# Kernel tuning notes

Hardware: AMD Instinct MI355X
Metric: run time of the kernel (lower is better)

## Reference

```python
import jax, jax.numpy as jnp
import numpy as np

N = 50000      # total nodes across batched subgraphs
E = 800000     # total edges
R = 4          # num_relations
G = 16         # number of graphs (questions) in batch
NODE_DIM = 128
QDIM = 768
RQ = 64        # reduced_qn_dim
RN = 64        # reduced_node_dim
H = 128        # hidden_dim
OUT = 64       # output_dim


def setup_inputs() -> dict:
    key = jax.random.key(0)
    ks = jax.random.split(key, 16)
    def lin(k, i, o):
        return jax.random.normal(k, (i, o), jnp.float32) / np.float32(np.sqrt(i))
    def rel(k, i, o):
        return jax.random.normal(k, (R, i, o), jnp.float32) / np.float32(np.sqrt(i))
    return {
        "x": jax.random.normal(ks[0], (N, NODE_DIM), jnp.float32),
        "edge_index": jax.random.randint(ks[1], (2, E), 0, N, dtype=jnp.int32),
        "edge_attr": jax.random.randint(ks[2], (E,), 0, R, dtype=jnp.int32),
        "batch": jnp.sort(jax.random.randint(ks[3], (N,), 0, G, dtype=jnp.int32)),
        "question_embedding": jax.random.normal(ks[4], (G, QDIM), jnp.float32),
        "qn_W": lin(ks[5], QDIM, RQ), "qn_b": jnp.zeros((RQ,), jnp.float32),
        "W0": rel(ks[6], NODE_DIM, RN), "root0": lin(ks[7], NODE_DIM, RN), "b0": jnp.zeros((RN,), jnp.float32),
        "W1": rel(ks[8], RN + RQ, H), "root1": lin(ks[9], RN + RQ, H), "b1": jnp.zeros((H,), jnp.float32),
        "W2": rel(ks[10], H, H), "root2": lin(ks[11], H, H), "b2": jnp.zeros((H,), jnp.float32),
        "W3": rel(ks[12], H, OUT), "root3": lin(ks[13], H, OUT), "b3": jnp.zeros((OUT,), jnp.float32),
    }


def rgcn_conv(x, src, dst, etype, W, root, b):
    """PyG RGCNConv: out_i = x_i @ root + b + sum_r mean_{j in N_r(i)} x_j @ W_r."""
    out = x @ root + b
    for r in range(R):
        h = x @ W[r]                                  # [N, out] transform-then-gather
        mask = (etype == r)
        msgs = jnp.where(mask[:, None], h[src], 0.0)  # [E, out]
        s = jax.ops.segment_sum(msgs, dst, num_segments=N)
        cnt = jax.ops.segment_sum(mask.astype(x.dtype), dst, num_segments=N)
        out = out + s / jnp.maximum(cnt, 1.0)[:, None]
    return out


def reference(x, edge_index, edge_attr, batch, question_embedding,
              qn_W, qn_b, W0, root0, b0, W1, root1, b1, W2, root2, b2, W3, root3, b3):
    src, dst = edge_index[0], edge_index[1]
    q = jax.nn.relu(question_embedding @ qn_W + qn_b)          # [G, RQ]
    h = jax.nn.relu(rgcn_conv(x, src, dst, edge_attr, W0, root0, b0))
    combined = jnp.concatenate([h, q[batch]], axis=1)          # [N, RN+RQ]
    h = jax.nn.relu(rgcn_conv(combined, src, dst, edge_attr, W1, root1, b1))
    h = jax.nn.relu(rgcn_conv(h, src, dst, edge_attr, W2, root2, b2))
    return rgcn_conv(h, src, dst, edge_attr, W3, root3, b3)
```

## Files before the change

kernel.cpp:

```cpp
#include <hip/hip_runtime.h>
#include <hip/hip_bf16.h>

#define NN 50000
#define EE 800000
#define GG 16
#define QD 768
#define NBUCK 196
#define EPB 4000

#define AGG_GRID 2048
#define AGG_STRIDE (AGG_GRID * 4)

typedef __bf16 bf16x8 __attribute__((ext_vector_type(8)));
typedef float f32x4 __attribute__((ext_vector_type(4)));
typedef int v4i __attribute__((ext_vector_type(4)));

extern "C" __device__ int __llvm_amdgcn_raw_buffer_load_i32(v4i rsrc, int voffset,
                                                            int soffset, int aux)
    __asm("llvm.amdgcn.raw.buffer.load.i32");

static __device__ __forceinline__ float bflo(unsigned u) {
    union { unsigned v; float f; } c; c.v = u << 16; return c.f;
}
static __device__ __forceinline__ float bfhi(unsigned u) {
    union { unsigned v; float f; } c; c.v = u & 0xffff0000u; return c.f;
}


#define PB_CVT 6250
#define PB_W0  (PB_CVT + 160)
#define PB_W1  (PB_W0 + 320)
#define PB_W2  (PB_W1 + 320)
#define PB_W3  (PB_W2 + 160)
#define PB_Q   (PB_W3 + 16)
#define PB_Z   (PB_Q + 1)
#define PB_HIST (PB_Z + 256)

__global__ __launch_bounds__(256) void prep_hist(
        const float* __restrict__ x, __hip_bfloat16* __restrict__ xb0e,
        __hip_bfloat16* __restrict__ xb1e,
        const float* __restrict__ qe, const float* __restrict__ qn_W,
        const float* __restrict__ qn_b, float* __restrict__ q,
        const float* __restrict__ W0, const float* __restrict__ root0, __hip_bfloat16* __restrict__ W5T0,
        const float* __restrict__ W1, const float* __restrict__ root1, __hip_bfloat16* __restrict__ W5T1,
        const float* __restrict__ W2, const float* __restrict__ root2, __hip_bfloat16* __restrict__ W5T2,
        const float* __restrict__ W3, const float* __restrict__ root3, __hip_bfloat16* __restrict__ W5T3,
        const int* __restrict__ edst, int* __restrict__ bcnt) {
    __shared__ float red[256];
    int blk = blockIdx.x, tid = threadIdx.x;
    if (blk < PB_CVT) {
        int i = blk * 256 + tid;
        float4 v = ((const float4*)x)[i];
        union { ushort4 u; __hip_bfloat16 h[4]; } o;
        o.h[0] = __float2bfloat16(v.x); o.h[1] = __float2bfloat16(v.y);
        o.h[2] = __float2bfloat16(v.z); o.h[3] = __float2bfloat16(v.w);
        ((ushort4*)xb0e)[i] = o.u;
    } else if (blk < PB_W3) {
        const float* W; const float* root; __hip_bfloat16* WT; int O, base;
        if (blk < PB_W0)      { W = W0; root = root0; WT = W5T0; O = 64;  base = PB_CVT; }
        else if (blk < PB_W1) { W = W1; root = root1; WT = W5T1; O = 128; base = PB_W0; }
        else if (blk < PB_W2) { W = W2; root = root2; WT = W5T2; O = 128; base = PB_W1; }
        else                  { W = W3; root = root3; WT = W5T3; O = 64;  base = PB_W2; }
        int idx = (blk - base) * 256 + tid;
        int o = idx / 640, k = idx - o * 640;
        float v;
        if (k < 128) v = root[(size_t)k * O + o];
        else { int r = (k - 128) >> 7, kk = (k - 128) & 127; v = W[((size_t)r * 128 + kk) * O + o]; }
        WT[idx] = __float2bfloat16(v);
    } else if (blk < PB_Q) {
        int g = blk - PB_W3;
        int o = tid & 63, kc = tid >> 6;
        const float* qr = qe + (size_t)g * QD;
        float s = 0.f;
        int k0 = kc * 192;
        for (int k = k0; k < k0 + 192; ++k)
            s = fmaf(qr[k], qn_W[(size_t)k * 64 + o], s);
        red[tid] = s;
        __syncthreads();
        if (tid < 64) {
            float t = red[tid] + red[tid + 64] + red[tid + 128] + red[tid + 192] + qn_b[o];
            q[g * 64 + o] = fmaxf(t, 0.f);
        }
    } else if (blk < PB_Z) {
        if (tid < 64) {
            ((unsigned*)((char*)xb0e + (size_t)NN * 256))[tid] = 0u;
            ((unsigned*)((char*)xb1e + (size_t)NN * 256))[tid] = 0u;
        }
    } else {
        __shared__ int h[NBUCK];
        int hb = blk - PB_Z;
        for (int i = tid; i < NBUCK; i += 256) h[i] = 0;
        __syncthreads();
        for (int e = hb * 256 + tid; e < EE; e += 256 * 256)
            atomicAdd(&h[edst[e] >> 8], 1);
        __syncthreads();
        for (int i = tid; i < NBUCK; i += 256) if (h[i]) atomicAdd(&bcnt[i], h[i]);
    }
}


__global__ void bucket_scan(const int* __restrict__ bcnt, int* __restrict__ bbase,
                            int* __restrict__ bcur) {
    __shared__ int wt[4];
    int tid = threadIdx.x, lane = tid & 63, w = tid >> 6;
    int v = (tid < NBUCK) ? bcnt[tid] : 0;
    int sc = v;
#pragma unroll
    for (int off = 1; off < 64; off <<= 1) {
        int t = __shfl_up(sc, off, 64);
        if (lane >= off) sc += t;
    }
    if (lane == 63) wt[w] = sc;
    __syncthreads();
    int wbase = 0;
    for (int ww = 0; ww < w; ++ww) wbase += wt[ww];
    int excl = wbase + sc - v;
    if (tid <= NBUCK) bbase[tid] = excl;
    if (tid < NBUCK) bcur[tid] = excl;
}

__global__ __launch_bounds__(256) void bin_edges(const int* __restrict__ src,
                                                 const int* __restrict__ dst,
                                                 const int* __restrict__ et,
                                                 int* __restrict__ bcur,
                                                 unsigned* __restrict__ binned) {
    __shared__ int lcnt[NBUCK];
    __shared__ int lbase[NBUCK];
    int tid = threadIdx.x;
    int e0 = blockIdx.x * EPB, e1 = min(e0 + EPB, EE);
    for (int base = e0; base < e1; base += 2048) {
        for (int i = tid; i < NBUCK; i += 256) lcnt[i] = 0;
        __syncthreads();
        unsigned ent[8]; int bk[8], rk[8];
#pragma unroll
        for (int k = 0; k < 8; ++k) {
            int e = base + k * 256 + tid;
            if (e < e1) {
                int d = dst[e];
                bk[k] = d >> 8;
                ent[k] = ((unsigned)src[e] << 10) | ((unsigned)et[e] << 8) | (unsigned)(d & 255);
                rk[k] = atomicAdd(&lcnt[bk[k]], 1);
            } else bk[k] = -1;
        }
        __syncthreads();
        for (int i = tid; i < NBUCK; i += 256)
            lbase[i] = lcnt[i] ? atomicAdd(&bcur[i], lcnt[i]) : 0;
        __syncthreads();
#pragma unroll
        for (int k = 0; k < 8; ++k)
            if (bk[k] >= 0) binned[lbase[bk[k]] + rk[k]] = ent[k];
        __syncthreads();
    }
}

__global__ __launch_bounds__(256) void csr_fine(const int* __restrict__ bbase,
                                                const unsigned* __restrict__ binned,
                                                int* __restrict__ csr,
                                                int* __restrict__ offsets,
                                                int4* __restrict__ cnt4) {
    __shared__ int cnt[1024];
    __shared__ int wt[4];
    int b = blockIdx.x, tid = threadIdx.x, lane = tid & 63, w = tid >> 6;
    int seg0 = bbase[b], seg1 = bbase[b + 1];
    for (int i = tid; i < 1024; i += 256) cnt[i] = 0;
    __syncthreads();
    for (int e = seg0 + tid; e < seg1; e += 256) {
        unsigned u = binned[e];
        atomicAdd(&cnt[(u & 255) * 4 + ((u >> 8) & 3)], 1);
    }
    __syncthreads();
    int c0 = cnt[tid * 4], c1 = cnt[tid * 4 + 1], c2 = cnt[tid * 4 + 2], c3 = cnt[tid * 4 + 3];
    int s = c0 + c1 + c2 + c3;
    int sc = s;
#pragma unroll
    for (int off = 1; off < 64; off <<= 1) {
        int t = __shfl_up(sc, off, 64);
        if (lane >= off) sc += t;
    }
    if (lane == 63) wt[w] = sc;
    __syncthreads();
    int wbase = 0;
    for (int ww = 0; ww < w; ++ww) wbase += wt[ww];
    int excl = wbase + sc - s;
    cnt[tid * 4]     = excl;
    cnt[tid * 4 + 1] = excl + c0;
    cnt[tid * 4 + 2] = excl + c0 + c1;
    cnt[tid * 4 + 3] = excl + c0 + c1 + c2;
    int node = b * 256 + tid;
    if (node < NN) {
        offsets[node] = seg0 + excl;
        cnt4[node] = make_int4(c0, c1, c2, c3);
    }
    if (b == NBUCK - 1 && tid == 0) offsets[NN] = EE;
    __syncthreads();
    for (int e = seg0 + tid; e < seg1; e += 256) {
        unsigned u = binned[e];
        int r = atomicAdd(&cnt[(u & 255) * 4 + ((u >> 8) & 3)], 1);
        csr[seg0 + r] = (int)(((u >> 10) << 2) | ((u >> 8) & 3));
    }
}


__global__ __launch_bounds__(256) void agg_x(const __hip_bfloat16* __restrict__ X,
                                             const int* __restrict__ offsets,
                                             const int4* __restrict__ cnt4,
                                             const int* __restrict__ csr,
                                             __hip_bfloat16* __restrict__ X5agg) {
    int lane = threadIdx.x & 63;
    int gw = blockIdx.x * 4 + (threadIdx.x >> 6);
    int laneoff = lane * 4;

    v4i rsrc;
    rsrc.x = (int)(unsigned)(size_t)X;
    rsrc.y = (int)((size_t)X >> 32);
    rsrc.z = NN * 256;
    rsrc.w = 0x00020000;

    for (int n0 = gw; n0 < NN; n0 += AGG_STRIDE) {
        int node = __builtin_amdgcn_readfirstlane(n0);
        int e0 = __builtin_amdgcn_readfirstlane(offsets[node]);
        int4 c4 = cnt4[node];
        int cs0 = __builtin_amdgcn_readfirstlane(c4.x);
        int cs1 = __builtin_amdgcn_readfirstlane(c4.y);
        int cs2 = __builtin_amdgcn_readfirstlane(c4.z);
        int cs3 = __builtin_amdgcn_readfirstlane(c4.w);
        int st1 = cs0, st2 = st1 + cs1, st3 = st2 + cs2;
        int maxc = max(max(cs0, cs1), max(cs2, cs3));
        float aL[4] = {0.f, 0.f, 0.f, 0.f}, aH[4] = {0.f, 0.f, 0.f, 0.f};
        for (int base = 0; base < maxc; base += 64) {
            int pk0 = csr[min(e0 + base + lane, EE - 1)];
            int pk1 = csr[min(e0 + st1 + base + lane, EE - 1)];
            int pk2 = csr[min(e0 + st2 + base + lane, EE - 1)];
            int pk3 = csr[min(e0 + st3 + base + lane, EE - 1)];
            int mm = min(64, maxc - base);
            for (int j = 0; j < mm; j += 4) {
                unsigned u[16];
#pragma unroll
                for (int jj = 0; jj < 4; ++jj) {
                    int i = base + j + jj;
                    int sl = j + jj;
                    int s0 = (i < cs0) ? ((__builtin_amdgcn_readlane(pk0, sl) >> 2) << 8) : 0x7F000000;
                    int s1 = (i < cs1) ? ((__builtin_amdgcn_readlane(pk1, sl) >> 2) << 8) : 0x7F000000;
                    int s2 = (i < cs2) ? ((__builtin_amdgcn_readlane(pk2, sl) >> 2) << 8) : 0x7F000000;
                    int s3 = (i < cs3) ? ((__builtin_amdgcn_readlane(pk3, sl) >> 2) << 8) : 0x7F000000;
                    u[jj * 4 + 0] = (unsigned)__llvm_amdgcn_raw_buffer_load_i32(rsrc, laneoff, s0, 0);
                    u[jj * 4 + 1] = (unsigned)__llvm_amdgcn_raw_buffer_load_i32(rsrc, laneoff, s1, 0);
                    u[jj * 4 + 2] = (unsigned)__llvm_amdgcn_raw_buffer_load_i32(rsrc, laneoff, s2, 0);
                    u[jj * 4 + 3] = (unsigned)__llvm_amdgcn_raw_buffer_load_i32(rsrc, laneoff, s3, 0);
                }
#pragma unroll
                for (int k = 0; k < 16; ++k) {
                    int r = k & 3;
                    aL[r] += bflo(u[k]);
                    aH[r] += bfhi(u[k]);
                }
            }
        }
        char* x5 = (char*)X5agg;
        int csa[4] = {cs0, cs1, cs2, cs3};
#pragma unroll
        for (int r = 0; r < 4; ++r) {
            float iv = 1.f / fmaxf((float)csa[r], 1.f);
            __hip_bfloat16 g0 = __float2bfloat16(aL[r] * iv);
            __hip_bfloat16 g1 = __float2bfloat16(aH[r] * iv);
            ushort2 pkd;
            pkd.x = *(unsigned short*)&g0; pkd.y = *(unsigned short*)&g1;
            *(ushort2*)(x5 + (size_t)node * 1024 + r * 256 + lane * 4) = pkd;
        }
    }
}


template <int O, int MODE>
__global__ __launch_bounds__(256) void dense5(const __hip_bfloat16* __restrict__ Xself,
                                              const __hip_bfloat16* __restrict__ X5agg,
                                              const __hip_bfloat16* __restrict__ W5T,
                                              const float* __restrict__ bias,
                                              const float* __restrict__ q,
                                              const int* __restrict__ batch,
                                              __hip_bfloat16* __restrict__ xnext,
                                              float* __restrict__ out) {
    __shared__ char lds[16384];
    constexpr int NCT = O / 16;
    int tid = threadIdx.x;
    int wave = tid >> 6, lane = tid & 63;
    int quad = lane >> 4, l15 = lane & 15;
    int mbase = blockIdx.x * 128 + wave * 32;
    const __bf16* Ws = (const __bf16*)W5T;

    f32x4 acc[2][NCT];
#pragma unroll
    for (int mt = 0; mt < 2; ++mt)
#pragma unroll
        for (int t = 0; t < NCT; ++t) acc[mt][t] = f32x4{0, 0, 0, 0};

    int arow0 = min(mbase + l15, NN - 1);
    int arow1 = min(mbase + 16 + l15, NN - 1);
    const __bf16* aps0 = (const __bf16*)Xself + (size_t)arow0 * 128;
    const __bf16* aps1 = (const __bf16*)Xself + (size_t)arow1 * 128;
    const __bf16* apg0 = (const __bf16*)X5agg + (size_t)arow0 * 512;
    const __bf16* apg1 = (const __bf16*)X5agg + (size_t)arow1 * 512;

    for (int kc = 0; kc < 10; ++kc) {
        int k0 = kc * 64;
        const __bf16* a0base = (kc < 2) ? aps0 + kc * 64 : apg0 + (kc - 2) * 64;
        const __bf16* a1base = (kc < 2) ? aps1 + kc * 64 : apg1 + (kc - 2) * 64;
        __syncthreads();
        constexpr int NF = NCT * 2 * 64;
#pragma unroll
        for (int i = 0; i < NF / 256; ++i) {
            int f = tid + i * 256;
            int fl = f & 63;
            int o = (f >> 7) * 16 + (fl & 15);
            int kk = k0 + ((f >> 6) & 1) * 32 + ((fl >> 4) & 3) * 8;
            *(uint4*)(lds + f * 16) = *(const uint4*)(Ws + (size_t)o * 640 + kk);
        }
        __syncthreads();
#pragma unroll
        for (int ks = 0; ks < 2; ++ks) {
            bf16x8 a0 = *(const bf16x8*)(a0base + ks * 32 + quad * 8);
            bf16x8 a1 = *(const bf16x8*)(a1base + ks * 32 + quad * 8);
#pragma unroll
            for (int t = 0; t < NCT; ++t) {
                bf16x8 b = *(const bf16x8*)(lds + ((t * 2 + ks) * 64 + lane) * 16);
                acc[0][t] = __builtin_amdgcn_mfma_f32_16x16x32_bf16(a0, b, acc[0][t], 0, 0, 0);
                acc[1][t] = __builtin_amdgcn_mfma_f32_16x16x32_bf16(a1, b, acc[1][t], 0, 0, 0);
            }
        }
    }
    __syncthreads();

    if (MODE == 2) {
#pragma unroll
        for (int mt = 0; mt < 2; ++mt)
#pragma unroll
            for (int t = 0; t < NCT; ++t) {
                int col = t * 16 + l15;
                float bv = bias[col];
#pragma unroll
                for (int reg = 0; reg < 4; ++reg) {
                    int row = mbase + mt * 16 + quad * 4 + reg;
                    if (row < NN) out[(size_t)row * 64 + col] = acc[mt][t][reg] + bv;
                }
            }
        return;
    }

    __hip_bfloat16* tp = (__hip_bfloat16*)(lds + wave * 4096);
#pragma unroll
    for (int mt = 0; mt < 2; ++mt) {
        int m0 = mbase + mt * 16;
#pragma unroll
        for (int t = 0; t < NCT; ++t) {
            int col = t * 16 + l15;
            float bv = bias[col];
#pragma unroll
            for (int reg = 0; reg < 4; ++reg)
                tp[(quad * 4 + reg) * 128 + col] =
                    __float2bfloat16(fmaxf(acc[mt][t][reg] + bv, 0.f));
        }
        if (MODE == 0) {
            int row = lane >> 2;
            int cs = (lane & 3) * 16;
            int rnode = min(m0 + row, NN - 1);
            int g = batch[rnode];
#pragma unroll
            for (int i = 0; i < 4; ++i) {
                float4 v = *(const float4*)(q + g * 64 + cs + i * 4);
                __hip_bfloat16 q0 = __float2bfloat16(v.x), q1 = __float2bfloat16(v.y);
                __hip_bfloat16 q2 = __float2bfloat16(v.z), q3 = __float2bfloat16(v.w);
                ushort4 pk;
                pk.x = *(unsigned short*)&q0; pk.y = *(unsigned short*)&q1;
                pk.z = *(unsigned short*)&q2; pk.w = *(unsigned short*)&q3;
                *(ushort4*)(tp + row * 128 + 64 + cs + i * 4) = pk;
            }
        }
#pragma unroll
        for (int p = 0; p < 4; ++p) {
            int c = p * 64 + lane;
            int row = m0 + (c >> 4);
            if (row < NN)
                *(uint4*)((char*)xnext + (size_t)row * 256 + (c & 15) * 16) =
                    *(const uint4*)((const char*)tp + c * 16);
        }
    }
}


static inline size_t rup(size_t x) { return (x + 255) & ~(size_t)255; }

extern "C" void kernel_launch(void* const* d_in, const int* in_sizes, int n_in,
                              void* d_out, int out_size, void* d_ws, size_t ws_size,
                              hipStream_t stream) {
    const float* x      = (const float*)d_in[0];
    const int*   esrc   = (const int*)d_in[1];
    const int*   edst   = esrc + EE;
    const int*   eattr  = (const int*)d_in[2];
    const int*   batch  = (const int*)d_in[3];
    const float* qe     = (const float*)d_in[4];
    const float* qn_W   = (const float*)d_in[5];
    const float* qn_b   = (const float*)d_in[6];
    const float* W0 = (const float*)d_in[7],  *root0 = (const float*)d_in[8],  *b0 = (const float*)d_in[9];
    const float* W1 = (const float*)d_in[10], *root1 = (const float*)d_in[11], *b1 = (const float*)d_in[12];
    const float* W2 = (const float*)d_in[13], *root2 = (const float*)d_in[14], *b2 = (const float*)d_in[15];
    const float* W3 = (const float*)d_in[16], *root3 = (const float*)d_in[17], *b3 = (const float*)d_in[18];
    float* out = (float*)d_out;

    char* w = (char*)d_ws;
    float* q       = (float*)w;  w += rup(GG * 64 * 4);
    int*   offsets = (int*)w;    w += rup(((size_t)NN + 1) * 4);
    int4*  cnt4    = (int4*)w;   w += rup((size_t)NN * 16);
    int*   bcnt    = (int*)w;    w += rup((size_t)NBUCK * 4);
    int*   bbase   = (int*)w;    w += rup(((size_t)NBUCK + 1) * 4);
    int*   bcur    = (int*)w;    w += rup((size_t)NBUCK * 4);
    unsigned* binned = (unsigned*)w; w += rup((size_t)EE * 4);
    int*   csr     = (int*)w;    w += rup((size_t)EE * 4);
    __hip_bfloat16* W5T0 = (__hip_bfloat16*)w; w += rup((size_t)64 * 640 * 2);
    __hip_bfloat16* W5T1 = (__hip_bfloat16*)w; w += rup((size_t)128 * 640 * 2);
    __hip_bfloat16* W5T2 = (__hip_bfloat16*)w; w += rup((size_t)128 * 640 * 2);
    __hip_bfloat16* W5T3 = (__hip_bfloat16*)w; w += rup((size_t)64 * 640 * 2);
    __hip_bfloat16* xb0 = (__hip_bfloat16*)w;  w += rup(((size_t)NN + 1) * 128 * 2);
    __hip_bfloat16* xb1 = (__hip_bfloat16*)w;  w += rup(((size_t)NN + 1) * 128 * 2);
    __hip_bfloat16* X5  = (__hip_bfloat16*)w;  w += rup((size_t)NN * 512 * 2);

    hipMemsetAsync(bcnt, 0, (size_t)NBUCK * 4, stream);

    prep_hist<<<PB_HIST, 256, 0, stream>>>(x, xb0, xb1, qe, qn_W, qn_b, q,
                                           W0, root0, W5T0, W1, root1, W5T1,
                                           W2, root2, W5T2, W3, root3, W5T3,
                                           edst, bcnt);

    bucket_scan<<<1, 256, 0, stream>>>(bcnt, bbase, bcur);
    bin_edges<<<(EE + EPB - 1) / EPB, 256, 0, stream>>>(esrc, edst, eattr, bcur, binned);
    csr_fine<<<NBUCK, 256, 0, stream>>>(bbase, binned, csr, offsets, cnt4);

    int dblk = (NN + 127) / 128;

    agg_x<<<AGG_GRID, 256, 0, stream>>>(xb0, offsets, cnt4, csr, X5);
    dense5<64, 0><<<dblk, 256, 0, stream>>>(xb0, X5, W5T0, b0, q, batch, xb1, nullptr);

    agg_x<<<AGG_GRID, 256, 0, stream>>>(xb1, offsets, cnt4, csr, X5);
    dense5<128, 1><<<dblk, 256, 0, stream>>>(xb1, X5, W5T1, b1, nullptr, nullptr, xb0, nullptr);

    agg_x<<<AGG_GRID, 256, 0, stream>>>(xb0, offsets, cnt4, csr, X5);
    dense5<128, 1><<<dblk, 256, 0, stream>>>(xb0, X5, W5T2, b2, nullptr, nullptr, xb1, nullptr);

    agg_x<<<AGG_GRID, 256, 0, stream>>>(xb1, offsets, cnt4, csr, X5);
    dense5<64, 2><<<dblk, 256, 0, stream>>>(xb1, X5, W5T3, b3, nullptr, nullptr, nullptr, out);
}
```

Before: 380.0 us.

## Split agg_x wave by relation with 16-byte gathers per lane

Restructures the per-node aggregation so each quarter-wave (16 lanes) handles one relation and each lane loads 16 bytes of a neighbor row via vector buffer loads, instead of every lane loading 4 bytes for all four relations. CSR indices are fetched per lane via buffer loads rather than readlane broadcasts, and the output is written as one 16-byte store per lane. This cuts instruction count and readlane/scalar overhead, and uses wider memory transactions. In exchange, the loop runs to the max relation count, so lanes of shorter relations sit idle, and serial dependent index loads per iteration may expose latency.

```diff
diff --git a/kernel.cpp b/kernel.cpp
--- a/kernel.cpp
+++ b/kernel.cpp
@@ -18,6 +18,9 @@
 extern "C" __device__ int __llvm_amdgcn_raw_buffer_load_i32(v4i rsrc, int voffset,
                                                             int soffset, int aux)
     __asm("llvm.amdgcn.raw.buffer.load.i32");
+extern "C" __device__ v4i __llvm_amdgcn_raw_buffer_load_v4i32(v4i rsrc, int voffset,
+                                                              int soffset, int aux)
+    __asm("llvm.amdgcn.raw.buffer.load.v4i32");
 
 static __device__ __forceinline__ float bflo(unsigned u) {
     union { unsigned v; float f; } c; c.v = u << 16; return c.f;
@@ -208,13 +211,18 @@
                                              __hip_bfloat16* __restrict__ X5agg) {
     int lane = threadIdx.x & 63;
     int gw = blockIdx.x * 4 + (threadIdx.x >> 6);
-    int laneoff = lane * 4;
-
-    v4i rsrc;
-    rsrc.x = (int)(unsigned)(size_t)X;
-    rsrc.y = (int)((size_t)X >> 32);
-    rsrc.z = NN * 256;
-    rsrc.w = 0x00020000;
+    int r = lane >> 4;
+    int chunk = (lane & 15) * 16;
+
+    v4i xsrd, csrd;
+    xsrd.x = (int)(unsigned)(size_t)X;
+    xsrd.y = (int)((size_t)X >> 32);
+    xsrd.z = NN * 256;
+    xsrd.w = 0x00020000;
+    csrd.x = (int)(unsigned)(size_t)csr;
+    csrd.y = (int)((size_t)csr >> 32);
+    csrd.z = EE * 4;
+    csrd.w = 0x00020000;
 
     for (int n0 = gw; n0 < NN; n0 += AGG_STRIDE) {
         int node = __builtin_amdgcn_readfirstlane(n0);
@@ -224,49 +232,39 @@
         int cs1 = __builtin_amdgcn_readfirstlane(c4.y);
         int cs2 = __builtin_amdgcn_readfirstlane(c4.z);
         int cs3 = __builtin_amdgcn_readfirstlane(c4.w);
-        int st1 = cs0, st2 = st1 + cs1, st3 = st2 + cs2;
         int maxc = max(max(cs0, cs1), max(cs2, cs3));
-        float aL[4] = {0.f, 0.f, 0.f, 0.f}, aH[4] = {0.f, 0.f, 0.f, 0.f};
-        for (int base = 0; base < maxc; base += 64) {
-            int pk0 = csr[min(e0 + base + lane, EE - 1)];
-            int pk1 = csr[min(e0 + st1 + base + lane, EE - 1)];
-            int pk2 = csr[min(e0 + st2 + base + lane, EE - 1)];
-            int pk3 = csr[min(e0 + st3 + base + lane, EE - 1)];
-            int mm = min(64, maxc - base);
-            for (int j = 0; j < mm; j += 4) {
-                unsigned u[16];
-#pragma unroll
-                for (int jj = 0; jj < 4; ++jj) {
-                    int i = base + j + jj;
-                    int sl = j + jj;
-                    int s0 = (i < cs0) ? ((__builtin_amdgcn_readlane(pk0, sl) >> 2) << 8) : 0x7F000000;
-                    int s1 = (i < cs1) ? ((__builtin_amdgcn_readlane(pk1, sl) >> 2) << 8) : 0x7F000000;
-                    int s2 = (i < cs2) ? ((__builtin_amdgcn_readlane(pk2, sl) >> 2) << 8) : 0x7F000000;
-                    int s3 = (i < cs3) ? ((__builtin_amdgcn_readlane(pk3, sl) >> 2) << 8) : 0x7F000000;
-                    u[jj * 4 + 0] = (unsigned)__llvm_amdgcn_raw_buffer_load_i32(rsrc, laneoff, s0, 0);
-                    u[jj * 4 + 1] = (unsigned)__llvm_amdgcn_raw_buffer_load_i32(rsrc, laneoff, s1, 0);
-                    u[jj * 4 + 2] = (unsigned)__llvm_amdgcn_raw_buffer_load_i32(rsrc, laneoff, s2, 0);
-                    u[jj * 4 + 3] = (unsigned)__llvm_amdgcn_raw_buffer_load_i32(rsrc, laneoff, s3, 0);
-                }
-#pragma unroll
-                for (int k = 0; k < 16; ++k) {
-                    int r = k & 3;
-                    aL[r] += bflo(u[k]);
-                    aH[r] += bfhi(u[k]);
-                }
+        int st_v = ((r >= 1) ? cs0 : 0) + ((r >= 2) ? cs1 : 0) + ((r >= 3) ? cs2 : 0);
+        int cs_v = (r == 0) ? cs0 : ((r == 1) ? cs1 : ((r == 2) ? cs2 : cs3));
+        int basev = (e0 + st_v) * 4;
+
+        float aF[8] = {0.f, 0.f, 0.f, 0.f, 0.f, 0.f, 0.f, 0.f};
+
+        for (int i = 0; i < maxc; i += 2) {
+            int pkA = __llvm_amdgcn_raw_buffer_load_i32(csrd, basev, i * 4, 0);
+            int pkB = __llvm_amdgcn_raw_buffer_load_i32(csrd, basev, i * 4 + 4, 0);
+            int vA = ((pkA >> 2) << 8) + chunk;
+            int vB = ((pkB >> 2) << 8) + chunk;
+            vA = (i < cs_v) ? vA : 0x7F000000;
+            vB = (i + 1 < cs_v) ? vB : 0x7F000000;
+            v4i uA = __llvm_amdgcn_raw_buffer_load_v4i32(xsrd, vA, 0, 0);
+            v4i uB = __llvm_amdgcn_raw_buffer_load_v4i32(xsrd, vB, 0, 0);
+#pragma unroll
+            for (int d = 0; d < 4; ++d) {
+                aF[d * 2]     += bflo((unsigned)uA[d]);
+                aF[d * 2 + 1] += bfhi((unsigned)uA[d]);
+                aF[d * 2]     += bflo((unsigned)uB[d]);
+                aF[d * 2 + 1] += bfhi((unsigned)uB[d]);
             }
         }
-        char* x5 = (char*)X5agg;
-        int csa[4] = {cs0, cs1, cs2, cs3};
-#pragma unroll
-        for (int r = 0; r < 4; ++r) {
-            float iv = 1.f / fmaxf((float)csa[r], 1.f);
-            __hip_bfloat16 g0 = __float2bfloat16(aL[r] * iv);
-            __hip_bfloat16 g1 = __float2bfloat16(aH[r] * iv);
-            ushort2 pkd;
-            pkd.x = *(unsigned short*)&g0; pkd.y = *(unsigned short*)&g1;
-            *(ushort2*)(x5 + (size_t)node * 1024 + r * 256 + lane * 4) = pkd;
-        }
+
+        float iv = 1.f / fmaxf((float)cs_v, 1.f);
+        union { uint4 u; unsigned short h[8]; } o;
+#pragma unroll
+        for (int d = 0; d < 8; ++d) {
+            __hip_bfloat16 g = __float2bfloat16(aF[d] * iv);
+            o.h[d] = *(unsigned short*)&g;
+        }
+        *(uint4*)((char*)X5agg + (size_t)node * 1024 + lane * 16) = o.u;
     }
 }
 
```

Measured after the change: 376.2 us. Within noise of the previous version (-1.0%).

## Switch RGCN layers from aggregate-then-transform to transform-then-gather

Applied to the files above, without the earlier changes.

Each layer now first runs a dense MFMA GEMM producing root and per-relation transformed rows (5*O columns) into HT. A gather kernel then sums scaled transformed rows per destination over the CSR, applying mean normalisation, bias, ReLU and the question concat in its epilogue. This removes the K=640 dense pass and the 1 KB-per-node aggregated buffer. For the O=64 layers it also halves the bytes gathered per edge, though the HT intermediate is larger than before.

```diff
diff --git a/kernel.cpp b/kernel.cpp
--- a/kernel.cpp
+++ b/kernel.cpp
@@ -33,18 +33,16 @@
 #define PB_W2  (PB_W1 + 320)
 #define PB_W3  (PB_W2 + 160)
 #define PB_Q   (PB_W3 + 16)
-#define PB_Z   (PB_Q + 1)
-#define PB_HIST (PB_Z + 256)
+#define PB_HIST (PB_Q + 256)
 
 __global__ __launch_bounds__(256) void prep_hist(
-        const float* __restrict__ x, __hip_bfloat16* __restrict__ xb0e,
-        __hip_bfloat16* __restrict__ xb1e,
+        const float* __restrict__ x, __hip_bfloat16* __restrict__ xb0,
         const float* __restrict__ qe, const float* __restrict__ qn_W,
         const float* __restrict__ qn_b, float* __restrict__ q,
-        const float* __restrict__ W0, const float* __restrict__ root0, __hip_bfloat16* __restrict__ W5T0,
-        const float* __restrict__ W1, const float* __restrict__ root1, __hip_bfloat16* __restrict__ W5T1,
-        const float* __restrict__ W2, const float* __restrict__ root2, __hip_bfloat16* __restrict__ W5T2,
-        const float* __restrict__ W3, const float* __restrict__ root3, __hip_bfloat16* __restrict__ W5T3,
+        const float* __restrict__ W0, const float* __restrict__ root0, __hip_bfloat16* __restrict__ WT0,
+        const float* __restrict__ W1, const float* __restrict__ root1, __hip_bfloat16* __restrict__ WT1,
+        const float* __restrict__ W2, const float* __restrict__ root2, __hip_bfloat16* __restrict__ WT2,
+        const float* __restrict__ W3, const float* __restrict__ root3, __hip_bfloat16* __restrict__ WT3,
         const int* __restrict__ edst, int* __restrict__ bcnt) {
     __shared__ float red[256];
     int blk = blockIdx.x, tid = threadIdx.x;
@@ -54,18 +52,22 @@
         union { ushort4 u; __hip_bfloat16 h[4]; } o;
         o.h[0] = __float2bfloat16(v.x); o.h[1] = __float2bfloat16(v.y);
         o.h[2] = __float2bfloat16(v.z); o.h[3] = __float2bfloat16(v.w);
-        ((ushort4*)xb0e)[i] = o.u;
+        ((ushort4*)xb0)[i] = o.u;
     } else if (blk < PB_W3) {
-        const float* W; const float* root; __hip_bfloat16* WT; int O, base;
-        if (blk < PB_W0)      { W = W0; root = root0; WT = W5T0; O = 64;  base = PB_CVT; }
-        else if (blk < PB_W1) { W = W1; root = root1; WT = W5T1; O = 128; base = PB_W0; }
-        else if (blk < PB_W2) { W = W2; root = root2; WT = W5T2; O = 128; base = PB_W1; }
-        else                  { W = W3; root = root3; WT = W5T3; O = 64;  base = PB_W2; }
+        const float* W; const float* root; __hip_bfloat16* WT; int O, logO, base;
+        if (blk < PB_W0)      { W = W0; root = root0; WT = WT0; O = 64;  logO = 6; base = PB_CVT; }
+        else if (blk < PB_W1) { W = W1; root = root1; WT = WT1; O = 128; logO = 7; base = PB_W0; }
+        else if (blk < PB_W2) { W = W2; root = root2; WT = WT2; O = 128; logO = 7; base = PB_W1; }
+        else                  { W = W3; root = root3; WT = WT3; O = 64;  logO = 6; base = PB_W2; }
         int idx = (blk - base) * 256 + tid;
-        int o = idx / 640, k = idx - o * 640;
+        int og = idx >> 7, kk = idx & 127;
         float v;
-        if (k < 128) v = root[(size_t)k * O + o];
-        else { int r = (k - 128) >> 7, kk = (k - 128) & 127; v = W[((size_t)r * 128 + kk) * O + o]; }
+        if (og < O) v = root[(size_t)kk * O + og];
+        else {
+            int t2 = og - O;
+            int r = t2 >> logO, oo = t2 & (O - 1);
+            v = W[((size_t)r * 128 + kk) * O + oo];
+        }
         WT[idx] = __float2bfloat16(v);
     } else if (blk < PB_Q) {
         int g = blk - PB_W3;
@@ -81,14 +83,9 @@
             float t = red[tid] + red[tid + 64] + red[tid + 128] + red[tid + 192] + qn_b[o];
             q[g * 64 + o] = fmaxf(t, 0.f);
         }
-    } else if (blk < PB_Z) {
-        if (tid < 64) {
-            ((unsigned*)((char*)xb0e + (size_t)NN * 256))[tid] = 0u;
-            ((unsigned*)((char*)xb1e + (size_t)NN * 256))[tid] = 0u;
-        }
     } else {
         __shared__ int h[NBUCK];
-        int hb = blk - PB_Z;
+        int hb = blk - PB_Q;
         for (int i = tid; i < NBUCK; i += 256) h[i] = 0;
         __syncthreads();
         for (int e = hb * 256 + tid; e < EE; e += 256 * 256)
@@ -201,20 +198,99 @@
 }
 
 
-__global__ __launch_bounds__(256) void agg_x(const __hip_bfloat16* __restrict__ X,
-                                             const int* __restrict__ offsets,
-                                             const int4* __restrict__ cnt4,
-                                             const int* __restrict__ csr,
-                                             __hip_bfloat16* __restrict__ X5agg) {
-    int lane = threadIdx.x & 63;
-    int gw = blockIdx.x * 4 + (threadIdx.x >> 6);
-    int laneoff = lane * 4;
-
-    v4i rsrc;
-    rsrc.x = (int)(unsigned)(size_t)X;
-    rsrc.y = (int)((size_t)X >> 32);
-    rsrc.z = NN * 256;
-    rsrc.w = 0x00020000;
+template <int OC5>
+__global__ __launch_bounds__(256) void denseT(const __hip_bfloat16* __restrict__ X,
+                                              const __hip_bfloat16* __restrict__ WT,
+                                              __hip_bfloat16* __restrict__ HT) {
+    __shared__ char lds[20480];
+    constexpr int NCT = 10;
+    constexpr int NCTILES = OC5 / 160;
+    int tid = threadIdx.x, wave = tid >> 6, lane = tid & 63;
+    int quad = lane >> 4, l15 = lane & 15;
+    int ct = blockIdx.x % NCTILES, rt = blockIdx.x / NCTILES;
+    int mbase = rt * 128 + wave * 32;
+    int cbase = ct * 160;
+    const __bf16* Ws = (const __bf16*)WT;
+
+    f32x4 acc[2][NCT];
+#pragma unroll
+    for (int mt = 0; mt < 2; ++mt)
+#pragma unroll
+        for (int t = 0; t < NCT; ++t) acc[mt][t] = f32x4{0, 0, 0, 0};
+
+    int arow0 = min(mbase + l15, NN - 1);
+    int arow1 = min(mbase + 16 + l15, NN - 1);
+    const __bf16* ap0 = (const __bf16*)X + (size_t)arow0 * 128;
+    const __bf16* ap1 = (const __bf16*)X + (size_t)arow1 * 128;
+
+    for (int kc = 0; kc < 2; ++kc) {
+        int k0 = kc * 64;
+        __syncthreads();
+#pragma unroll
+        for (int i = 0; i < 5; ++i) {
+            int f = tid + i * 256;
+            int fl = f & 63;
+            int t = f >> 7;
+            int ks = (f >> 6) & 1;
+            int og = cbase + t * 16 + (fl & 15);
+            int kk = k0 + ks * 32 + ((fl >> 4) & 3) * 8;
+            *(uint4*)(lds + f * 16) = *(const uint4*)(Ws + (size_t)og * 128 + kk);
+        }
+        __syncthreads();
+#pragma unroll
+        for (int ks = 0; ks < 2; ++ks) {
+            bf16x8 a0 = *(const bf16x8*)(ap0 + k0 + ks * 32 + quad * 8);
+            bf16x8 a1 = *(const bf16x8*)(ap1 + k0 + ks * 32 + quad * 8);
+#pragma unroll
+            for (int t = 0; t < NCT; ++t) {
+                bf16x8 b = *(const bf16x8*)(lds + ((t * 2 + ks) * 64 + lane) * 16);
+                acc[0][t] = __builtin_amdgcn_mfma_f32_16x16x32_bf16(a0, b, acc[0][t], 0, 0, 0);
+                acc[1][t] = __builtin_amdgcn_mfma_f32_16x16x32_bf16(a1, b, acc[1][t], 0, 0, 0);
+            }
+        }
+    }
+    __syncthreads();
+
+    __hip_bfloat16* tp = (__hip_bfloat16*)(lds + wave * 5120);
+    for (int mt = 0; mt < 2; ++mt) {
+        int m0 = mbase + mt * 16;
+#pragma unroll
+        for (int t = 0; t < NCT; ++t) {
+            int col = t * 16 + l15;
+#pragma unroll
+            for (int reg = 0; reg < 4; ++reg)
+                tp[(quad * 4 + reg) * 160 + col] = __float2bfloat16(acc[mt][t][reg]);
+        }
+#pragma unroll
+        for (int p = 0; p < 5; ++p) {
+            int b = p * 1024 + lane * 16;
+            int row = b / 320;
+            int cb = b - row * 320;
+            if (m0 + row < NN)
+                *(uint4*)((char*)HT + (size_t)(m0 + row) * (OC5 * 2) + cbase * 2 + cb) =
+                    *(const uint4*)((const char*)tp + b);
+        }
+    }
+}
+
+
+template <int O, int MODE>
+__global__ __launch_bounds__(256) void gsum(const __hip_bfloat16* __restrict__ HT,
+        const int* __restrict__ offsets, const int4* __restrict__ cnt4,
+        const int* __restrict__ csr, const float* __restrict__ bias,
+        const float* __restrict__ q, const int* __restrict__ batch,
+        __hip_bfloat16* __restrict__ xnext, float* __restrict__ out) {
+    constexpr int STRIDE = 5 * O * 2;
+    constexpr int ROWB = O * 2;
+    int tid = threadIdx.x;
+    int lane = tid & 63;
+    int gw = blockIdx.x * 4 + (tid >> 6);
+
+    v4i hsrd, csrd;
+    hsrd.x = (int)(unsigned)(size_t)HT; hsrd.y = (int)((size_t)HT >> 32);
+    hsrd.z = NN * STRIDE; hsrd.w = 0x00020000;
+    csrd.x = (int)(unsigned)(size_t)csr; csrd.y = (int)((size_t)csr >> 32);
+    csrd.z = EE * 4; csrd.w = 0x00020000;
 
     for (int n0 = gw; n0 < NN; n0 += AGG_STRIDE) {
         int node = __builtin_amdgcn_readfirstlane(n0);
@@ -224,164 +300,106 @@
         int cs1 = __builtin_amdgcn_readfirstlane(c4.y);
         int cs2 = __builtin_amdgcn_readfirstlane(c4.z);
         int cs3 = __builtin_amdgcn_readfirstlane(c4.w);
-        int st1 = cs0, st2 = st1 + cs1, st3 = st2 + cs2;
-        int maxc = max(max(cs0, cs1), max(cs2, cs3));
-        float aL[4] = {0.f, 0.f, 0.f, 0.f}, aH[4] = {0.f, 0.f, 0.f, 0.f};
-        for (int base = 0; base < maxc; base += 64) {
-            int pk0 = csr[min(e0 + base + lane, EE - 1)];
-            int pk1 = csr[min(e0 + st1 + base + lane, EE - 1)];
-            int pk2 = csr[min(e0 + st2 + base + lane, EE - 1)];
-            int pk3 = csr[min(e0 + st3 + base + lane, EE - 1)];
-            int mm = min(64, maxc - base);
-            for (int j = 0; j < mm; j += 4) {
-                unsigned u[16];
-#pragma unroll
-                for (int jj = 0; jj < 4; ++jj) {
-                    int i = base + j + jj;
-                    int sl = j + jj;
-                    int s0 = (i < cs0) ? ((__builtin_amdgcn_readlane(pk0, sl) >> 2) << 8) : 0x7F000000;
-                    int s1 = (i < cs1) ? ((__builtin_amdgcn_readlane(pk1, sl) >> 2) << 8) : 0x7F000000;
-                    int s2 = (i < cs2) ? ((__builtin_amdgcn_readlane(pk2, sl) >> 2) << 8) : 0x7F000000;
-                    int s3 = (i < cs3) ? ((__builtin_amdgcn_readlane(pk3, sl) >> 2) << 8) : 0x7F000000;
-                    u[jj * 4 + 0] = (unsigned)__llvm_amdgcn_raw_buffer_load_i32(rsrc, laneoff, s0, 0);
-                    u[jj * 4 + 1] = (unsigned)__llvm_amdgcn_raw_buffer_load_i32(rsrc, laneoff, s1, 0);
-                    u[jj * 4 + 2] = (unsigned)__llvm_amdgcn_raw_buffer_load_i32(rsrc, laneoff, s2, 0);
-                    u[jj * 4 + 3] = (unsigned)__llvm_amdgcn_raw_buffer_load_i32(rsrc, laneoff, s3, 0);
-                }
-#pragma unroll
-                for (int k = 0; k < 16; ++k) {
-                    int r = k & 3;
-                    aL[r] += bflo(u[k]);
-                    aH[r] += bfhi(u[k]);
+        int tcnt = cs0 + cs1 + cs2 + cs3;
+        float inv0 = 1.f / (float)max(cs0, 1);
+        float inv1 = 1.f / (float)max(cs1, 1);
+        float inv2 = 1.f / (float)max(cs2, 1);
+        float inv3 = 1.f / (float)max(cs3, 1);
+        float a0 = 0.f, a1 = 0.f;
+
+        if (O == 128) {
+            for (int wb = 0; wb < tcnt; wb += 64) {
+                int pkw = __llvm_amdgcn_raw_buffer_load_i32(csrd, (e0 + wb + lane) * 4, 0, 0);
+                int m = min(64, tcnt - wb);
+                for (int j = 0; j < m; j += 4) {
+                    int sb[4]; float scv[4];
+#pragma unroll
+                    for (int k2 = 0; k2 < 4; ++k2) {
+                        int pk = __builtin_amdgcn_readlane(pkw, j + k2);
+                        int rel = pk & 3;
+                        scv[k2] = (rel & 2) ? ((rel & 1) ? inv3 : inv2)
+                                            : ((rel & 1) ? inv1 : inv0);
+                        sb[k2] = (j + k2 < m) ? ((pk >> 2) * STRIDE + (rel + 1) * ROWB)
+                                              : 0x7F000000;
+                    }
+                    unsigned u[4];
+#pragma unroll
+                    for (int k2 = 0; k2 < 4; ++k2)
+                        u[k2] = (unsigned)__llvm_amdgcn_raw_buffer_load_i32(hsrd, lane * 4, sb[k2], 0);
+#pragma unroll
+                    for (int k2 = 0; k2 < 4; ++k2) {
+                        a0 += scv[k2] * bflo(u[k2]);
+                        a1 += scv[k2] * bfhi(u[k2]);
+                    }
                 }
             }
-        }
-        char* x5 = (char*)X5agg;
-        int csa[4] = {cs0, cs1, cs2, cs3};
-#pragma unroll
-        for (int r = 0; r < 4; ++r) {
-            float iv = 1.f / fmaxf((float)csa[r], 1.f);
-            __hip_bfloat16 g0 = __float2bfloat16(aL[r] * iv);
-            __hip_bfloat16 g1 = __float2bfloat16(aH[r] * iv);
-            ushort2 pkd;
-            pkd.x = *(unsigned short*)&g0; pkd.y = *(unsigned short*)&g1;
-            *(ushort2*)(x5 + (size_t)node * 1024 + r * 256 + lane * 4) = pkd;
-        }
-    }
-}
-
-
-template <int O, int MODE>
-__global__ __launch_bounds__(256) void dense5(const __hip_bfloat16* __restrict__ Xself,
-                                              const __hip_bfloat16* __restrict__ X5agg,
-                                              const __hip_bfloat16* __restrict__ W5T,
-                                              const float* __restrict__ bias,
-                                              const float* __restrict__ q,
-                                              const int* __restrict__ batch,
-                                              __hip_bfloat16* __restrict__ xnext,
-                                              float* __restrict__ out) {
-    __shared__ char lds[16384];
-    constexpr int NCT = O / 16;
-    int tid = threadIdx.x;
-    int wave = tid >> 6, lane = tid & 63;
-    int quad = lane >> 4, l15 = lane & 15;
-    int mbase = blockIdx.x * 128 + wave * 32;
-    const __bf16* Ws = (const __bf16*)W5T;
-
-    f32x4 acc[2][NCT];
-#pragma unroll
-    for (int mt = 0; mt < 2; ++mt)
-#pragma unroll
-        for (int t = 0; t < NCT; ++t) acc[mt][t] = f32x4{0, 0, 0, 0};
-
-    int arow0 = min(mbase + l15, NN - 1);
-    int arow1 = min(mbase + 16 + l15, NN - 1);
-    const __bf16* aps0 = (const __bf16*)Xself + (size_t)arow0 * 128;
-    const __bf16* aps1 = (const __bf16*)Xself + (size_t)arow1 * 128;
-    const __bf16* apg0 = (const __bf16*)X5agg + (size_t)arow0 * 512;
-    const __bf16* apg1 = (const __bf16*)X5agg + (size_t)arow1 * 512;
-
-    for (int kc = 0; kc < 10; ++kc) {
-        int k0 = kc * 64;
-        const __bf16* a0base = (kc < 2) ? aps0 + kc * 64 : apg0 + (kc - 2) * 64;
-        const __bf16* a1base = (kc < 2) ? aps1 + kc * 64 : apg1 + (kc - 2) * 64;
-        __syncthreads();
-        constexpr int NF = NCT * 2 * 64;
-#pragma unroll
-        for (int i = 0; i < NF / 256; ++i) {
-            int f = tid + i * 256;
-            int fl = f & 63;
-            int o = (f >> 7) * 16 + (fl & 15);
-            int kk = k0 + ((f >> 6) & 1) * 32 + ((fl >> 4) & 3) * 8;
-            *(uint4*)(lds + f * 16) = *(const uint4*)(Ws + (size_t)o * 640 + kk);
-        }
-        __syncthreads();
-#pragma unroll
-        for (int ks = 0; ks < 2; ++ks) {
-            bf16x8 a0 = *(const bf16x8*)(a0base + ks * 32 + quad * 8);
-            bf16x8 a1 = *(const bf16x8*)(a1base + ks * 32 + quad * 8);
-#pragma unroll
-            for (int t = 0; t < NCT; ++t) {
-                bf16x8 b = *(const bf16x8*)(lds + ((t * 2 + ks) * 64 + lane) * 16);
-                acc[0][t] = __builtin_amdgcn_mfma_f32_16x16x32_bf16(a0, b, acc[0][t], 0, 0, 0);
-                acc[1][t] = __builtin_amdgcn_mfma_f32_16x16x32_bf16(a1, b, acc[1][t], 0, 0, 0);
-            }
-        }
-    }
-    __syncthreads();
-
-    if (MODE == 2) {
-#pragma unroll
-        for (int mt = 0; mt < 2; ++mt)
-#pragma unroll
-            for (int t = 0; t < NCT; ++t) {
-                int col = t * 16 + l15;
-                float bv = bias[col];
-#pragma unroll
-                for (int reg = 0; reg < 4; ++reg) {
-                    int row = mbase + mt * 16 + quad * 4 + reg;
-                    if (row < NN) out[(size_t)row * 64 + col] = acc[mt][t][reg] + bv;
+        } else {
+            int colb = (lane & 31) * 4;
+            bool hi_half = lane >= 32;
+            for (int wb = 0; wb < tcnt; wb += 64) {
+                int pkw = __llvm_amdgcn_raw_buffer_load_i32(csrd, (e0 + wb + lane) * 4, 0, 0);
+                int m = min(64, tcnt - wb);
+                for (int j = 0; j < m; j += 4) {
+                    int sbs[4]; float scs[4];
+#pragma unroll
+                    for (int k2 = 0; k2 < 4; ++k2) {
+                        int pk = __builtin_amdgcn_readlane(pkw, j + k2);
+                        int rel = pk & 3;
+                        scs[k2] = (rel & 2) ? ((rel & 1) ? inv3 : inv2)
+                                            : ((rel & 1) ? inv1 : inv0);
+                        sbs[k2] = (j + k2 < m) ? ((pk >> 2) * STRIDE + (rel + 1) * ROWB)
+                                               : 0x7F000000;
+                    }
+                    float sc0 = hi_half ? scs[1] : scs[0];
+                    float sc1 = hi_half ? scs[3] : scs[2];
+                    int sb0 = hi_half ? sbs[1] : sbs[0];
+                    int sb1 = hi_half ? sbs[3] : sbs[2];
+                    unsigned u0 = (unsigned)__llvm_amdgcn_raw_buffer_load_i32(hsrd, sb0 + colb, 0, 0);
+                    unsigned u1 = (unsigned)__llvm_amdgcn_raw_buffer_load_i32(hsrd, sb1 + colb, 0, 0);
+                    a0 += sc0 * bflo(u0) + sc1 * bflo(u1);
+                    a1 += sc0 * bfhi(u0) + sc1 * bfhi(u1);
                 }
             }
-        return;
-    }
-
-    __hip_bfloat16* tp = (__hip_bfloat16*)(lds + wave * 4096);
-#pragma unroll
-    for (int mt = 0; mt < 2; ++mt) {
-        int m0 = mbase + mt * 16;
-#pragma unroll
-        for (int t = 0; t < NCT; ++t) {
-            int col = t * 16 + l15;
-            float bv = bias[col];
-#pragma unroll
-            for (int reg = 0; reg < 4; ++reg)
-                tp[(quad * 4 + reg) * 128 + col] =
-                    __float2bfloat16(fmaxf(acc[mt][t][reg] + bv, 0.f));
-        }
-        if (MODE == 0) {
-            int row = lane >> 2;
-            int cs = (lane & 3) * 16;
-            int rnode = min(m0 + row, NN - 1);
-            int g = batch[rnode];
-#pragma unroll
-            for (int i = 0; i < 4; ++i) {
-                float4 v = *(const float4*)(q + g * 64 + cs + i * 4);
-                __hip_bfloat16 q0 = __float2bfloat16(v.x), q1 = __float2bfloat16(v.y);
-                __hip_bfloat16 q2 = __float2bfloat16(v.z), q3 = __float2bfloat16(v.w);
-                ushort4 pk;
-                pk.x = *(unsigned short*)&q0; pk.y = *(unsigned short*)&q1;
-                pk.z = *(unsigned short*)&q2; pk.w = *(unsigned short*)&q3;
-                *(ushort4*)(tp + row * 128 + 64 + cs + i * 4) = pk;
+            a0 += __shfl_xor(a0, 32);
+            a1 += __shfl_xor(a1, 32);
+        }
+
+        if (MODE == 1) {
+            unsigned us = (unsigned)__llvm_amdgcn_raw_buffer_load_i32(hsrd, lane * 4, node * STRIDE, 0);
+            float2 bv = *(const float2*)(bias + lane * 2);
+            float o0 = fmaxf(bflo(us) + bv.x + a0, 0.f);
+            float o1 = fmaxf(bfhi(us) + bv.y + a1, 0.f);
+            __hip_bfloat16 h0 = __float2bfloat16(o0), h1 = __float2bfloat16(o1);
+            ushort2 pkd;
+            pkd.x = *(unsigned short*)&h0; pkd.y = *(unsigned short*)&h1;
+            *(ushort2*)((char*)xnext + (size_t)node * 256 + lane * 4) = pkd;
+        } else if (MODE == 0) {
+            if (lane < 32) {
+                unsigned us = (unsigned)__llvm_amdgcn_raw_buffer_load_i32(hsrd, lane * 4, node * STRIDE, 0);
+                float2 bv = *(const float2*)(bias + lane * 2);
+                float o0 = fmaxf(bflo(us) + bv.x + a0, 0.f);
+                float o1 = fmaxf(bfhi(us) + bv.y + a1, 0.f);
+                __hip_bfloat16 h0 = __float2bfloat16(o0), h1 = __float2bfloat16(o1);
+                ushort2 pkd;
+                pkd.x = *(unsigned short*)&h0; pkd.y = *(unsigned short*)&h1;
+                *(ushort2*)((char*)xnext + (size_t)node * 256 + lane * 4) = pkd;
+            } else {
+                int g = batch[node];
+                float2 qv = *(const float2*)(q + g * 64 + (lane - 32) * 2);
+                __hip_bfloat16 h0 = __float2bfloat16(qv.x), h1 = __float2bfloat16(qv.y);
+                ushort2 pkd;
+                pkd.x = *(unsigned short*)&h0; pkd.y = *(unsigned short*)&h1;
+                *(ushort2*)((char*)xnext + (size_t)node * 256 + 128 + (lane - 32) * 4) = pkd;
             }
-        }
-#pragma unroll
-        for (int p = 0; p < 4; ++p) {
-            int c = p * 64 + lane;
-            int row = m0 + (c >> 4);
-            if (row < NN)
-                *(uint4*)((char*)xnext + (size_t)row * 256 + (c & 15) * 16) =
-                    *(const uint4*)((const char*)tp + c * 16);
+        } else {
+            if (lane < 32) {
+                unsigned us = (unsigned)__llvm_amdgcn_raw_buffer_load_i32(hsrd, lane * 4, node * STRIDE, 0);
+                float2 bv = *(const float2*)(bias + lane * 2);
+                float2 ov;
+                ov.x = bflo(us) + bv.x + a0;
+                ov.y = bfhi(us) + bv.y + a1;
+                *(float2*)(out + (size_t)node * 64 + lane * 2) = ov;
+            }
         }
     }
 }
@@ -415,36 +433,36 @@
     int*   bcur    = (int*)w;    w += rup((size_t)NBUCK * 4);
     unsigned* binned = (unsigned*)w; w += rup((size_t)EE * 4);
     int*   csr     = (int*)w;    w += rup((size_t)EE * 4);
-    __hip_bfloat16* W5T0 = (__hip_bfloat16*)w; w += rup((size_t)64 * 640 * 2);
-    __hip_bfloat16* W5T1 = (__hip_bfloat16*)w; w += rup((size_t)128 * 640 * 2);
-    __hip_bfloat16* W5T2 = (__hip_bfloat16*)w; w += rup((size_t)128 * 640 * 2);
-    __hip_bfloat16* W5T3 = (__hip_bfloat16*)w; w += rup((size_t)64 * 640 * 2);
-    __hip_bfloat16* xb0 = (__hip_bfloat16*)w;  w += rup(((size_t)NN + 1) * 128 * 2);
-    __hip_bfloat16* xb1 = (__hip_bfloat16*)w;  w += rup(((size_t)NN + 1) * 128 * 2);
-    __hip_bfloat16* X5  = (__hip_bfloat16*)w;  w += rup((size_t)NN * 512 * 2);
+    __hip_bfloat16* WT0 = (__hip_bfloat16*)w; w += rup((size_t)320 * 128 * 2);
+    __hip_bfloat16* WT1 = (__hip_bfloat16*)w; w += rup((size_t)640 * 128 * 2);
+    __hip_bfloat16* WT2 = (__hip_bfloat16*)w; w += rup((size_t)640 * 128 * 2);
+    __hip_bfloat16* WT3 = (__hip_bfloat16*)w; w += rup((size_t)320 * 128 * 2);
+    __hip_bfloat16* xb0 = (__hip_bfloat16*)w;  w += rup((size_t)NN * 128 * 2);
+    __hip_bfloat16* xb1 = (__hip_bfloat16*)w;  w += rup((size_t)NN * 128 * 2);
+    __hip_bfloat16* HT  = (__hip_bfloat16*)w;  w += rup((size_t)NN * 640 * 2);
 
     hipMemsetAsync(bcnt, 0, (size_t)NBUCK * 4, stream);
 
-    prep_hist<<<PB_HIST, 256, 0, stream>>>(x, xb0, xb1, qe, qn_W, qn_b, q,
-                                           W0, root0, W5T0, W1, root1, W5T1,
-                                           W2, root2, W5T2, W3, root3, W5T3,
+    prep_hist<<<PB_HIST, 256, 0, stream>>>(x, xb0, qe, qn_W, qn_b, q,
+                                           W0, root0, WT0, W1, root1, WT1,
+                                           W2, root2, WT2, W3, root3, WT3,
                                            edst, bcnt);
 
     bucket_scan<<<1, 256, 0, stream>>>(bcnt, bbase, bcur);
     bin_edges<<<(EE + EPB - 1) / EPB, 256, 0, stream>>>(esrc, edst, eattr, bcur, binned);
     csr_fine<<<NBUCK, 256, 0, stream>>>(bbase, binned, csr, offsets, cnt4);
 
-    int dblk = (NN + 127) / 128;
-
-    agg_x<<<AGG_GRID, 256, 0, stream>>>(xb0, offsets, cnt4, csr, X5);
-    dense5<64, 0><<<dblk, 256, 0, stream>>>(xb0, X5, W5T0, b0, q, batch, xb1, nullptr);
-
-    agg_x<<<AGG_GRID, 256, 0, stream>>>(xb1, offsets, cnt4, csr, X5);
-    dense5<128, 1><<<dblk, 256, 0, stream>>>(xb1, X5, W5T1, b1, nullptr, nullptr, xb0, nullptr);
-
-    agg_x<<<AGG_GRID, 256, 0, stream>>>(xb0, offsets, cnt4, csr, X5);
-    dense5<128, 1><<<dblk, 256, 0, stream>>>(xb0, X5, W5T2, b2, nullptr, nullptr, xb1, nullptr);
-
-    agg_x<<<AGG_GRID, 256, 0, stream>>>(xb1, offsets, cnt4, csr, X5);
-    dense5<64, 2><<<dblk, 256, 0, stream>>>(xb1, X5, W5T3, b3, nullptr, nullptr, nullptr, out);
-}
+    int rowtiles = (NN + 127) / 128;
+
+    denseT<320><<<rowtiles * 2, 256, 0, stream>>>(xb0, WT0, HT);
+    gsum<64, 0><<<AGG_GRID, 256, 0, stream>>>(HT, offsets, cnt4, csr, b0, q, batch, xb1, nullptr);
+
+    denseT<640><<<rowtiles * 4, 256, 0, stream>>>(xb1, WT1, HT);
+    gsum<128, 1><<<AGG_GRID, 256, 0, stream>>>(HT, offsets, cnt4, csr, b1, nullptr, nullptr, xb0, nullptr);
+
+    denseT<640><<<rowtiles * 4, 256, 0, stream>>>(xb0, WT2, HT);
+    gsum<128, 1><<<AGG_GRID, 256, 0, stream>>>(HT, offsets, cnt4, csr, b2, nullptr, nullptr, xb1, nullptr);
+
+    denseT<320><<<rowtiles * 2, 256, 0, stream>>>(xb1, WT3, HT);
+    gsum<64, 2><<<AGG_GRID, 256, 0, stream>>>(HT, offsets, cnt4, csr, b3, nullptr, nullptr, nullptr, out);
+}
```

Result: slower. 420.8 us (+10.8%).
